# Kernel tuning notes

Measured on AMD Instinct MI355X. Metric: run time of the kernel, lower is better.

Reference implementation:

```python
import jax, jax.numpy as jnp
import numpy as np

N = 100000      # nodes
E = 1600000     # edges (before self-loops)
D_IN = 128      # node_attr_size
H = 4           # gat_heads
C = 32          # hidden_size (per-head out channels)
F = H * C       # feature_size = 128
K = 16          # num_clusters
L = 2           # num_gat_layers
EPS = 1e-5
NEG_SLOPE = 0.2  # PyG GATv2Conv default leaky_relu slope


def setup_inputs() -> dict:
    key = jax.random.key(0)
    ks = jax.random.split(key, 8)
    x = jax.random.normal(ks[0], (N, D_IN), jnp.float32)
    edge_index = jax.random.randint(ks[1], (2, E), 0, N, jnp.int32)
    sF = 1.0 / np.sqrt(F).astype(np.float32)
    Wp = jax.random.normal(ks[2], (D_IN, F), jnp.float32) * (1.0 / np.sqrt(D_IN).astype(np.float32))
    bp = jnp.zeros((F,), jnp.float32)
    ln_g = jnp.ones((L, F), jnp.float32)
    ln_b = jnp.zeros((L, F), jnp.float32)
    Wl = jax.random.normal(ks[3], (L, F, H * C), jnp.float32) * sF
    bl = jnp.zeros((L, H * C), jnp.float32)
    Wr = jax.random.normal(ks[4], (L, F, H * C), jnp.float32) * sF
    br = jnp.zeros((L, H * C), jnp.float32)
    att = jax.random.normal(ks[5], (L, H, C), jnp.float32) * (1.0 / np.sqrt(C).astype(np.float32))
    gb = jnp.zeros((L, F), jnp.float32)  # GATv2Conv output bias
    Wc = jax.random.normal(ks[6], (F, K), jnp.float32) * sF
    bc = jnp.zeros((K,), jnp.float32)
    return dict(x=x, edge_index=edge_index, Wp=Wp, bp=bp, ln_g=ln_g, ln_b=ln_b,
                Wl=Wl, bl=bl, Wr=Wr, br=br, att=att, gb=gb, Wc=Wc, bc=bc)


def _layernorm(x, g, b):
    mu = jnp.mean(x, axis=-1, keepdims=True)
    var = jnp.var(x, axis=-1, keepdims=True)
    return (x - mu) * jax.lax.rsqrt(var + EPS) * g + b


def reference(x, edge_index, Wp, bp, ln_g, ln_b, Wl, bl, Wr, br, att, gb, Wc, bc):
    # GATv2Conv adds self-loops by default
    loops = jnp.arange(N, dtype=edge_index.dtype)
    src = jnp.concatenate([edge_index[0], loops])  # message source j
    dst = jnp.concatenate([edge_index[1], loops])  # message target i

    h = x @ Wp + bp  # node_feat_proj -> [N, F]
    for i in range(L):
        identity = h
        hn = _layernorm(h, ln_g[i], ln_b[i])
        x_l = (hn @ Wl[i] + bl[i]).reshape(N, H, C)  # source transform
        x_r = (hn @ Wr[i] + br[i]).reshape(N, H, C)  # target transform
        m = x_l[src] + x_r[dst]                       # [E+N, H, C]
        s = jnp.where(m > 0, m, NEG_SLOPE * m)        # leaky_relu(0.2)
        logits = jnp.einsum('ehc,hc->eh', s, att[i])  # [E+N, H]
        # segment softmax over incoming edges of each target node
        mx = jax.ops.segment_max(logits, dst, num_segments=N)
        a = jnp.exp(logits - mx[dst])
        den = jax.ops.segment_sum(a, dst, num_segments=N)
        alpha = a / den[dst]
        out = jax.ops.segment_sum(x_l[src] * alpha[:, :, None], dst, num_segments=N)
        out = out.reshape(N, F) + gb[i]
        # relu activation, dropout identity (eval), residual add
        h = jax.nn.relu(out) + identity

    classification_output = h @ Wc + bc
    return (classification_output, h)
```

## Files before the change

kernel.cpp:

```cpp
#include <hip/hip_runtime.h>
#include <hip/hip_bf16.h>
#include <math.h>
#include <stdint.h>

#define N_NODES 100000
#define N_EDGES 1600000
#define ET (N_EDGES + N_NODES)
#define FDIM 128
#define NK 16
#define EPS 1e-5f
#define SLOPE 0.2f

typedef __attribute__((ext_vector_type(8))) short bf16x8;
typedef __attribute__((ext_vector_type(4))) float f32x4;
typedef __attribute__((ext_vector_type(2))) _Float16 h2;

__device__ inline unsigned pk_bf16(float a, float b) {
    float2 f; f.x = a; f.y = b;
    __hip_bfloat162 t = __float22bfloat162_rn(f);
    return *reinterpret_cast<unsigned*>(&t);
}
__device__ inline h2 as_h2(unsigned u) { return __builtin_bit_cast(h2, u); }
__device__ inline unsigned as_u(h2 v) { return __builtin_bit_cast(unsigned, v); }

#define SWZ(X, P) __int_as_float(__builtin_amdgcn_ds_swizzle(__float_as_int(X), (P)))
#define DPPF(X, CTRL) __int_as_float(__builtin_amdgcn_mov_dpp(__float_as_int(X), (CTRL), 0xF, 0xF, true))
#define DX1(X) DPPF(X, 0xB1)
#define DX2(X) DPPF(X, 0x4E)
#define DR4(X) DPPF(X, 0x124)
#define DR8(X) DPPF(X, 0x128)
#define DB0(X) DPPF(X, 0x00)
#define DB1(X) DPPF(X, 0x55)
#define DB2(X) DPPF(X, 0xAA)
#define DB3(X) DPPF(X, 0xFF)

__device__ inline float exp2_hw(float x) {
    float r;
    asm("v_exp_f32 %0, %1" : "=v"(r) : "v"(x));
    return r;
}

#define FMAMIX_LO(ACC, U, W) \
    asm("v_fma_mix_f32 %0, %1, %2, %0 op_sel_hi:[1,0,0]" : "+v"(ACC) : "v"(U), "v"(W))
#define FMAMIX_HI(ACC, U, W) \
    asm("v_fma_mix_f32 %0, %1, %2, %0 op_sel:[1,0,0] op_sel_hi:[1,0,0]" : "+v"(ACC) : "v"(U), "v"(W))

__device__ inline int rflm(int v) { return __builtin_amdgcn_readfirstlane(v) & 131071; }


#define NBKT 196
#define BSH 9
#define BSTRIDE 10240
#define P1_EPT 8
#define P1_EPB (256 * P1_EPT)
#define PART_BLOCKS ((ET + P1_EPB - 1) / P1_EPB)

__global__ __launch_bounds__(256) void prep_kernel(
        const int* __restrict__ ei, int* __restrict__ gcount,
        int* __restrict__ staging,
        const float* __restrict__ Wp, const float* __restrict__ Wl,
        const float* __restrict__ Wr, ushort* __restrict__ wbp,
        ushort* __restrict__ wbl0, ushort* __restrict__ wbl1) {
    __shared__ int hist[NBKT];
    __shared__ int lofs[NBKT];
    __shared__ int gbase[NBKT];
    __shared__ int s[256];
    __shared__ int spk[P1_EPB];
    __shared__ short sbk[P1_EPB];
    int bid = blockIdx.x;
    int t = threadIdx.x;
    if (bid >= PART_BLOCKS) {
        int bb = bid - PART_BLOCKS;
        const float *W0, *W1; ushort* out; int nt;
        if (bb < 8)       { W0 = Wp; W1 = Wp; out = wbp; nt = bb; }
        else if (bb < 24) { W0 = Wl; W1 = Wr; out = wbl0; nt = bb - 8; }
        else              { W0 = Wl + FDIM * FDIM; W1 = Wr + FDIM * FDIM; out = wbl1; nt = bb - 24; }
        int kk = t >> 6, lane = t & 63;
        int n = nt * 16 + (lane & 15);
        int k0 = kk * 32 + (lane >> 4) * 8;
        const float* W = (n < 128) ? (W0 + n) : (W1 + (n - 128));
        float f[8];
#pragma unroll
        for (int j = 0; j < 8; j++) f[j] = W[(size_t)(k0 + j) * FDIM];
        uint4 u;
        u.x = pk_bf16(f[0], f[1]); u.y = pk_bf16(f[2], f[3]);
        u.z = pk_bf16(f[4], f[5]); u.w = pk_bf16(f[6], f[7]);
        *(uint4*)&out[(size_t)((nt * 4 + kk) * 64 + lane) * 8] = u;
        return;
    }
    if (t < NBKT) hist[t] = 0;
    __syncthreads();
    int e0 = bid * P1_EPB + t;
    int pk[P1_EPT], bk[P1_EPT], rk[P1_EPT];
#pragma unroll
    for (int k = 0; k < P1_EPT; k++) {
        int e = e0 + k * 256;
        bk[k] = -1;
        if (e < ET) {
            int src, dst;
            if (e < N_EDGES) { src = ei[e]; dst = ei[N_EDGES + e]; }
            else             { src = dst = e - N_EDGES; }
            int b = dst >> BSH;
            pk[k] = (src << BSH) | (dst & 511);
            bk[k] = b;
            rk[k] = atomicAdd(&hist[b], 1);
        }
    }
    __syncthreads();
    int v = (t < NBKT) ? hist[t] : 0;
    s[t] = v;
    __syncthreads();
    for (int o = 1; o < 256; o <<= 1) {
        int add = (t >= o) ? s[t - o] : 0;
        __syncthreads();
        s[t] += add;
        __syncthreads();
    }
    if (t < NBKT) {
        lofs[t] = s[t] - v;
        gbase[t] = (v > 0) ? atomicAdd(&gcount[t], v) : 0;
    }
    __syncthreads();
#pragma unroll
    for (int k = 0; k < P1_EPT; k++) {
        if (bk[k] >= 0) {
            int idx = lofs[bk[k]] + rk[k];
            spk[idx] = pk[k];
            sbk[idx] = (short)bk[k];
        }
    }
    __syncthreads();
    int tot = lofs[NBKT - 1] + hist[NBKT - 1];
    for (int i = t; i < tot; i += 256) {
        int b = sbk[i];
        staging[b * BSTRIDE + gbase[b] + (i - lofs[b])] = spk[i];
    }
}

__global__ __launch_bounds__(256) void csr_projln_kernel(
        const int* __restrict__ staging, const int* __restrict__ gcount,
        int* __restrict__ off, int* __restrict__ perm,
        const float* __restrict__ x, const ushort* __restrict__ wb,
        const float* __restrict__ bp, float* __restrict__ h,
        const ushort* __restrict__ wbl,
        const float* __restrict__ g_, const float* __restrict__ b_,
        const float* __restrict__ bl, const float* __restrict__ br,
        ushort* __restrict__ xlh, ushort* __restrict__ xrh) {
    __shared__ uint4 fragbuf[4 * 272];
    int bid = blockIdx.x;
    int t = threadIdx.x;
    if (bid >= NBKT) {
        int wid = ((bid - NBKT) * 256 + t) >> 6;
        int lane = t & 63;
        if (wid >= N_NODES / 16) return;
        uint4* fb = fragbuf + (t >> 6) * 272;
        int q = lane >> 4, m = lane & 15;
        int row0 = wid * 16;
        const float* xrow = x + (size_t)(row0 + m) * FDIM + q * 32;
#pragma unroll
        for (int p = 0; p < 4; p++) {
            float4 a = *(const float4*)&xrow[p * 8];
            float4 c = *(const float4*)&xrow[p * 8 + 4];
            uint4 u;
            u.x = pk_bf16(a.x, a.y); u.y = pk_bf16(a.z, a.w);
            u.z = pk_bf16(c.x, c.y); u.w = pk_bf16(c.z, c.w);
            fb[q * 68 + p * 17 + m] = u;
        }
        bf16x8 A[4];
#pragma unroll
        for (int kk = 0; kk < 4; kk++)
            A[kk] = *(const bf16x8*)&fb[kk * 68 + q * 17 + m];
        const bf16x8* wbv = (const bf16x8*)wb;
        f32x4 acc[8];
        f32x4 z = {0.f, 0.f, 0.f, 0.f};
#pragma unroll
        for (int nt = 0; nt < 8; nt++) acc[nt] = z;
#pragma unroll
        for (int nt = 0; nt < 8; nt++) {
#pragma unroll
            for (int kk = 0; kk < 4; kk++) {
                bf16x8 B = wbv[(nt * 4 + kk) * 64 + lane];
                acc[nt] = __builtin_amdgcn_mfma_f32_16x16x32_bf16(A[kk], B, acc[nt], 0, 0, 0);
            }
        }
        float hv[8][4];
#pragma unroll
        for (int nt = 0; nt < 8; nt++) {
            int col = nt * 16 + m;
            float bias = bp[col];
#pragma unroll
            for (int r = 0; r < 4; r++) {
                hv[nt][r] = acc[nt][r] + bias;
                h[(size_t)(row0 + q * 4 + r) * FDIM + col] = hv[nt][r];
            }
        }
        if (!wbl) return;
        float gc[8], bcv[8];
#pragma unroll
        for (int nt = 0; nt < 8; nt++) { gc[nt] = g_[nt * 16 + m]; bcv[nt] = b_[nt * 16 + m]; }
        ushort* fbu = (ushort*)fb;
#pragma unroll
        for (int r = 0; r < 4; r++) {
            float s = 0.f, ss = 0.f;
#pragma unroll
            for (int nt = 0; nt < 8; nt++) { s += hv[nt][r]; ss += hv[nt][r] * hv[nt][r]; }
            s += SWZ(s, 0x041F); s += SWZ(s, 0x081F); s += SWZ(s, 0x101F); s += SWZ(s, 0x201F);
            ss += SWZ(ss, 0x041F); ss += SWZ(ss, 0x081F); ss += SWZ(ss, 0x101F); ss += SWZ(ss, 0x201F);
            float mu = s * (1.f / 128.f);
            float rv = rsqrtf(ss * (1.f / 128.f) - mu * mu + EPS);
#pragma unroll
            for (int nt = 0; nt < 8; nt++) {
                float val = (hv[nt][r] - mu) * rv * gc[nt] + bcv[nt];
                ushort us = (ushort)pk_bf16(val, val);
                fbu[(((nt >> 1) * 68 + ((nt & 1) * 2 + (m >> 3)) * 17 + (q * 4 + r)) << 3) + (m & 7)] = us;
            }
        }
        bf16x8 A2[4];
#pragma unroll
        for (int kk = 0; kk < 4; kk++)
            A2[kk] = *(const bf16x8*)&fb[kk * 68 + q * 17 + m];
        const bf16x8* wlv = (const bf16x8*)wbl;
        f32x4 acc2[16];
#pragma unroll
        for (int nt = 0; nt < 16; nt++) acc2[nt] = z;
#pragma unroll
        for (int nt = 0; nt < 16; nt++) {
#pragma unroll
            for (int kk = 0; kk < 4; kk++) {
                bf16x8 B = wlv[(nt * 4 + kk) * 64 + lane];
                acc2[nt] = __builtin_amdgcn_mfma_f32_16x16x32_bf16(A2[kk], B, acc2[nt], 0, 0, 0);
            }
        }
#pragma unroll
        for (int nt = 0; nt < 16; nt++) {
            int col = nt * 16 + m;
            if (nt < 8) {
                float bias = bl[col];
#pragma unroll
                for (int r = 0; r < 4; r++) {
                    _Float16 hf = (_Float16)(acc2[nt][r] + bias);
                    xlh[(size_t)(row0 + q * 4 + r) * FDIM + col] = __builtin_bit_cast(ushort, hf);
                }
            } else {
                int c2 = col - 128;
                float bias = br[c2];
#pragma unroll
                for (int r = 0; r < 4; r++) {
                    _Float16 hf = (_Float16)(acc2[nt][r] + bias);
                    xrh[(size_t)(row0 + q * 4 + r) * FDIM + c2] = __builtin_bit_cast(ushort, hf);
                }
            }
        }
        return;
    }
    int* hist = (int*)fragbuf;
    int* cur  = hist + 512;
    int* pr   = cur + 512;
    int* gpre = pr + 256;
    int b = bid;
    hist[t] = 0; hist[t + 256] = 0;
    gpre[t] = (t < NBKT) ? gcount[t] : 0;
    __syncthreads();
    int sz = gcount[b];
    for (int k = t; k < sz; k += 256)
        atomicAdd(&hist[staging[b * BSTRIDE + k] & 511], 1);
    __syncthreads();
    int a0 = hist[2 * t], a1 = hist[2 * t + 1];
    pr[t] = a0 + a1;
    __syncthreads();
    for (int o = 1; o < 256; o <<= 1) {
        int ad = (t >= o) ? pr[t - o] : 0;
        int gd = (t >= o) ? gpre[t - o] : 0;
        __syncthreads();
        pr[t] += ad;
        gpre[t] += gd;
        __syncthreads();
    }
    int base = gpre[b] - sz;
    int pe = pr[t] - (a0 + a1);
    cur[2 * t] = pe;
    cur[2 * t + 1] = pe + a0;
    int n = (b << BSH) + 2 * t;
    if (n < N_NODES)     off[n]     = base + pe;
    if (n + 1 < N_NODES) off[n + 1] = base + pe + a0;
    if (b == 0 && t == 0) off[N_NODES] = ET;
    __syncthreads();
    for (int k = t; k < sz; k += 256) {
        int p = staging[b * BSTRIDE + k];
        int slot = atomicAdd(&cur[p & 511], 1);
        perm[base + slot] = p >> BSH;
    }
}


__global__ __launch_bounds__(256) void ln_gemm2_kernel(
        const float* __restrict__ h,
        const float* __restrict__ g, const float* __restrict__ b,
        const ushort* __restrict__ wb, const float* __restrict__ bl,
        const float* __restrict__ br,
        ushort* __restrict__ xlh, ushort* __restrict__ xrh) {
    __shared__ uint4 fragbuf[4 * 272];
    int wid = (blockIdx.x * 256 + threadIdx.x) >> 6;
    int lane = threadIdx.x & 63;
    if (wid >= N_NODES / 16) return;
    uint4* fb = fragbuf + (threadIdx.x >> 6) * 272;
    int q = lane >> 4, m = lane & 15;
    int row0 = wid * 16;
    const float* hrow = h + (size_t)(row0 + m) * FDIM + q * 32;
    float v[32];
#pragma unroll
    for (int i = 0; i < 8; i++) {
        float4 t4 = *(const float4*)&hrow[i * 4];
        v[i * 4 + 0] = t4.x; v[i * 4 + 1] = t4.y; v[i * 4 + 2] = t4.z; v[i * 4 + 3] = t4.w;
    }
    float s = 0.f, ss = 0.f;
#pragma unroll
    for (int i = 0; i < 32; i++) { s += v[i]; ss += v[i] * v[i]; }
    s  += __shfl_xor(s, 16);  s  += __shfl_xor(s, 32);
    ss += __shfl_xor(ss, 16); ss += __shfl_xor(ss, 32);
    float mu = s * (1.f / 128.f);
    float var = ss * (1.f / 128.f) - mu * mu;
    float rv = rsqrtf(var + EPS);
#pragma unroll
    for (int i = 0; i < 8; i++) {
        float4 gv = *(const float4*)&g[q * 32 + i * 4];
        float4 bv = *(const float4*)&b[q * 32 + i * 4];
        v[i * 4 + 0] = (v[i * 4 + 0] - mu) * rv * gv.x + bv.x;
        v[i * 4 + 1] = (v[i * 4 + 1] - mu) * rv * gv.y + bv.y;
        v[i * 4 + 2] = (v[i * 4 + 2] - mu) * rv * gv.z + bv.z;
        v[i * 4 + 3] = (v[i * 4 + 3] - mu) * rv * gv.w + bv.w;
    }
#pragma unroll
    for (int p = 0; p < 4; p++) {
        uint4 u;
        u.x = pk_bf16(v[p * 8 + 0], v[p * 8 + 1]);
        u.y = pk_bf16(v[p * 8 + 2], v[p * 8 + 3]);
        u.z = pk_bf16(v[p * 8 + 4], v[p * 8 + 5]);
        u.w = pk_bf16(v[p * 8 + 6], v[p * 8 + 7]);
        fb[q * 68 + p * 17 + m] = u;
    }
    bf16x8 A[4];
#pragma unroll
    for (int kk = 0; kk < 4; kk++)
        A[kk] = *(const bf16x8*)&fb[kk * 68 + q * 17 + m];
    const bf16x8* wbv = (const bf16x8*)wb;
    f32x4 acc[16];
    f32x4 z = {0.f, 0.f, 0.f, 0.f};
#pragma unroll
    for (int nt = 0; nt < 16; nt++) acc[nt] = z;
#pragma unroll
    for (int nt = 0; nt < 16; nt++) {
#pragma unroll
        for (int kk = 0; kk < 4; kk++) {
            bf16x8 B = wbv[(nt * 4 + kk) * 64 + lane];
            acc[nt] = __builtin_amdgcn_mfma_f32_16x16x32_bf16(A[kk], B, acc[nt], 0, 0, 0);
        }
    }
#pragma unroll
    for (int nt = 0; nt < 16; nt++) {
        int col = nt * 16 + m;
        if (nt < 8) {
            float bias = bl[col];
#pragma unroll
            for (int r = 0; r < 4; r++) {
                _Float16 hf = (_Float16)(acc[nt][r] + bias);
                xlh[(size_t)(row0 + q * 4 + r) * FDIM + col] = __builtin_bit_cast(ushort, hf);
            }
        } else {
            int c2 = col - 128;
            float bias = br[c2];
#pragma unroll
            for (int r = 0; r < 4; r++) {
                _Float16 hf = (_Float16)(acc[nt][r] + bias);
                xrh[(size_t)(row0 + q * 4 + r) * FDIM + c2] = __builtin_bit_cast(ushort, hf);
            }
        }
    }
}


__global__ __launch_bounds__(256) void gat_agg_kernel(
        const unsigned* __restrict__ xlp, const unsigned* __restrict__ xrp,
        const int* __restrict__ off, const int* __restrict__ perm,
        const float* __restrict__ att, const float* __restrict__ gb,
        float* __restrict__ h,
        const float* __restrict__ Wc, const float* __restrict__ bc,
        float* __restrict__ out_cls) {
    __shared__ float WcS[FDIM * NK];
    __shared__ float hbuf[4 * 256];
    bool dofinal = (Wc != nullptr);
    if (dofinal) {
        for (int i = threadIdx.x; i < FDIM * NK; i += 256) WcS[i] = Wc[i];
        __syncthreads();
    }
    int wave = (blockIdx.x * 256 + threadIdx.x) >> 6;
    unsigned lane = threadIdx.x & 63;
    int iA = wave * 2;
    int iB = iA + 1;
    int2 oA = *(const int2*)&off[iA];
    int eB2 = off[iB + 1];
    h2 xrvA = as_h2(xrp[(unsigned)iA * 64u + lane]);
    h2 xrvB = as_h2(xrp[(unsigned)iB * 64u + lane]);
    const float2 hidA = *(const float2*)&h[(size_t)iA * FDIM + lane * 2];
    const float2 hidB = *(const float2*)&h[(size_t)iB * FDIM + lane * 2];
    const float2 gbv = *(const float2*)&gb[lane * 2];
    float2 attf = *(const float2*)&att[lane * 2];
    h2 attp; attp[0] = (_Float16)(attf.x * 1.44269504f);
    attp[1] = (_Float16)(attf.y * 1.44269504f);
    const h2 c06 = {(_Float16)0.6f, (_Float16)0.6f};
    const h2 c04 = {(_Float16)0.4f, (_Float16)0.4f};
    bool b0 = lane & 1, b1 = lane & 2;
    int begA = __builtin_amdgcn_readfirstlane(oA.x);
    int endA = __builtin_amdgcn_readfirstlane(oA.y);
    int begB = endA;
    int endB = __builtin_amdgcn_readfirstlane(eB2);
    const char* xlB_ = (const char*)xlp;
    unsigned laneB = lane << 2;

#define GLD(J) (*(const unsigned*)(xlB_ + ((unsigned)(J) * 256u + laneB)))

#define EDGE_PARTIAL(XRV, U, T)                                     \
    {                                                               \
        h2 mm = as_h2(U) + XRV;                                     \
        h2 am = as_h2(as_u(mm) & 0x7FFF7FFFu);                      \
        h2 sv = am * c04 + mm * c06;                                \
        T = __builtin_amdgcn_fdot2(sv, attp, 0.f, false);           \
    }

#define COMPUTE4(S, U0, U1, U2, U3)                                 \
    {                                                               \
        float t0, t1, t2, t3;                                       \
        EDGE_PARTIAL(xrv##S, U0, t0);                               \
        EDGE_PARTIAL(xrv##S, U1, t1);                               \
        EDGE_PARTIAL(xrv##S, U2, t2);                               \
        EDGE_PARTIAL(xrv##S, U3, t3);                               \
        float u   = b0 ? t1 : t0;                                   \
        float uu2 = b0 ? t0 : t1;                                   \
        u += DX1(uu2);                                              \
        float vv  = b0 ? t3 : t2;                                   \
        float vv2 = b0 ? t2 : t3;                                   \
        vv += DX1(vv2);                                             \
        float ww  = b1 ? vv : u;                                    \
        float ww2 = b1 ? u : vv;                                    \
        ww += DX2(ww2);                                             \
        ww += DR4(ww);                                              \
        ww += DR8(ww);                                              \
        float ew = exp2_hw(ww);                                     \
        dloc##S += ew;                                              \
        float w0 = DB0(ew);                                         \
        float w1 = DB1(ew);                                         \
        float w2 = DB2(ew);                                         \
        float w3 = DB3(ew);                                         \
        FMAMIX_LO(accx##S, U0, w0); FMAMIX_HI(accy##S, U0, w0);     \
        FMAMIX_LO(accx##S, U1, w1); FMAMIX_HI(accy##S, U1, w1);     \
        FMAMIX_LO(accx##S, U2, w2); FMAMIX_HI(accy##S, U2, w2);     \
        FMAMIX_LO(accx##S, U3, w3); FMAMIX_HI(accy##S, U3, w3);     \
    }

#define TAIL1(S, U)                                                 \
    {                                                               \
        float tt;                                                   \
        EDGE_PARTIAL(xrv##S, U, tt);                                \
        tt += DX1(tt);                                              \
        tt += DX2(tt);                                              \
        tt += DR4(tt);                                              \
        tt += DR8(tt);                                              \
        float w = exp2_hw(tt);                                      \
        if ((lane & 3) == 0) dloc##S += w;                          \
        FMAMIX_LO(accx##S, U, w); FMAMIX_HI(accy##S, U, w);         \
    }

    int nbA = (endA - begA) >> 2, tlA = (endA - begA) & 3;
    int nbB = (endB - begB) >> 2, tlB = (endB - begB) & 3;
    float accxA = 0.f, accyA = 0.f, dlocA = 0.f;
    float accxB = 0.f, accyB = 0.f, dlocB = 0.f;
    unsigned c0A, c1A, c2A, c3A, d0A, d1A, d2A, d3A; int4 p2A;
    unsigned c0B, c1B, c2B, c3B, d0B, d1B, d2B, d3B; int4 p2B;
    unsigned t0A = 0, t1A = 0, t2A = 0, t0B = 0, t1B = 0, t2B = 0;
    int4 p0A, p1A, ptA, p0B, p1B, ptB;

    if (nbA > 0) {
        __builtin_memcpy(&p0A, perm + begA, 16);
        __builtin_memcpy(&p1A, perm + begA + 4, 16);
        __builtin_memcpy(&p2A, perm + begA + 8, 16);
    }
    if (tlA > 0) __builtin_memcpy(&ptA, perm + begA + 4 * nbA, 16);
    if (nbB > 0) {
        __builtin_memcpy(&p0B, perm + begB, 16);
        __builtin_memcpy(&p1B, perm + begB + 4, 16);
        __builtin_memcpy(&p2B, perm + begB + 8, 16);
    }
    if (tlB > 0) __builtin_memcpy(&ptB, perm + begB + 4 * nbB, 16);
    if (nbA > 0) {
        c0A = GLD(rflm(p0A.x)); c1A = GLD(rflm(p0A.y)); c2A = GLD(rflm(p0A.z)); c3A = GLD(rflm(p0A.w));
        d0A = GLD(rflm(p1A.x)); d1A = GLD(rflm(p1A.y)); d2A = GLD(rflm(p1A.z)); d3A = GLD(rflm(p1A.w));
    }
    if (nbB > 0) {
        c0B = GLD(rflm(p0B.x)); c1B = GLD(rflm(p0B.y)); c2B = GLD(rflm(p0B.z)); c3B = GLD(rflm(p0B.w));
        d0B = GLD(rflm(p1B.x)); d1B = GLD(rflm(p1B.y)); d2B = GLD(rflm(p1B.z)); d3B = GLD(rflm(p1B.w));
    }
    if (tlA > 0) {
        t0A = GLD(rflm(ptA.x));
        if (tlA > 1) t1A = GLD(rflm(ptA.y));
        if (tlA > 2) t2A = GLD(rflm(ptA.z));
    }
    if (tlB > 0) {
        t0B = GLD(rflm(ptB.x));
        if (tlB > 1) t1B = GLD(rflm(ptB.y));
        if (tlB > 2) t2B = GLD(rflm(ptB.z));
    }

    int blkA = 0, blkB = 0;
    while (blkA + 2 < nbA && blkB + 2 < nbB) {
        unsigned e0 = GLD(rflm(p2A.x)), e1 = GLD(rflm(p2A.y));
        unsigned e2 = GLD(rflm(p2A.z)), e3 = GLD(rflm(p2A.w));
        unsigned f0 = GLD(rflm(p2B.x)), f1 = GLD(rflm(p2B.y));
        unsigned f2 = GLD(rflm(p2B.z)), f3 = GLD(rflm(p2B.w));
        __builtin_memcpy(&p2A, perm + begA + 4 * blkA + 12, 16);
        __builtin_memcpy(&p2B, perm + begB + 4 * blkB + 12, 16);
        COMPUTE4(A, c0A, c1A, c2A, c3A);
        c0A = d0A; c1A = d1A; c2A = d2A; c3A = d3A;
        d0A = e0; d1A = e1; d2A = e2; d3A = e3;
        COMPUTE4(B, c0B, c1B, c2B, c3B);
        c0B = d0B; c1B = d1B; c2B = d2B; c3B = d3B;
        d0B = f0; d1B = f1; d2B = f2; d3B = f3;
        ++blkA; ++blkB;
    }
    for (; blkA + 2 < nbA; ++blkA) {
        unsigned e0 = GLD(rflm(p2A.x)), e1 = GLD(rflm(p2A.y));
        unsigned e2 = GLD(rflm(p2A.z)), e3 = GLD(rflm(p2A.w));
        __builtin_memcpy(&p2A, perm + begA + 4 * blkA + 12, 16);
        COMPUTE4(A, c0A, c1A, c2A, c3A);
        c0A = d0A; c1A = d1A; c2A = d2A; c3A = d3A;
        d0A = e0; d1A = e1; d2A = e2; d3A = e3;
    }
    for (; blkB + 2 < nbB; ++blkB) {
        unsigned f0 = GLD(rflm(p2B.x)), f1 = GLD(rflm(p2B.y));
        unsigned f2 = GLD(rflm(p2B.z)), f3 = GLD(rflm(p2B.w));
        __builtin_memcpy(&p2B, perm + begB + 4 * blkB + 12, 16);
        COMPUTE4(B, c0B, c1B, c2B, c3B);
        c0B = d0B; c1B = d1B; c2B = d2B; c3B = d3B;
        d0B = f0; d1B = f1; d2B = f2; d3B = f3;
    }
    if (nbA >= 2) {
        COMPUTE4(A, c0A, c1A, c2A, c3A);
        c0A = d0A; c1A = d1A; c2A = d2A; c3A = d3A;
    }
    if (nbB >= 2) {
        COMPUTE4(B, c0B, c1B, c2B, c3B);
        c0B = d0B; c1B = d1B; c2B = d2B; c3B = d3B;
    }
    if (nbA >= 1) COMPUTE4(A, c0A, c1A, c2A, c3A);
    if (nbB >= 1) COMPUTE4(B, c0B, c1B, c2B, c3B);
    if (tlA > 0) {
        TAIL1(A, t0A);
        if (tlA > 1) TAIL1(A, t1A);
        if (tlA > 2) TAIL1(A, t2A);
    }
    if (tlB > 0) {
        TAIL1(B, t0B);
        if (tlB > 1) TAIL1(B, t1B);
        if (tlB > 2) TAIL1(B, t2B);
    }
#undef EDGE_PARTIAL
#undef COMPUTE4
#undef TAIL1
#undef GLD

    float denA = dlocA + DX1(dlocA);
    denA += DX2(denA);
    float invA = 1.f / denA;
    float2 resA;
    resA.x = fmaxf(accxA * invA + gbv.x, 0.f) + hidA.x;
    resA.y = fmaxf(accyA * invA + gbv.y, 0.f) + hidA.y;
    *(float2*)&h[(size_t)iA * FDIM + lane * 2] = resA;
    float denB = dlocB + DX1(dlocB);
    denB += DX2(denB);
    float invB = 1.f / denB;
    float2 resB;
    resB.x = fmaxf(accxB * invB + gbv.x, 0.f) + hidB.x;
    resB.y = fmaxf(accyB * invB + gbv.y, 0.f) + hidB.y;
    *(float2*)&h[(size_t)iB * FDIM + lane * 2] = resB;

    if (dofinal) {
        float* sh = hbuf + (threadIdx.x >> 6) * 256;
        sh[lane * 2]       = resA.x; sh[lane * 2 + 1]       = resA.y;
        sh[128 + lane * 2] = resB.x; sh[128 + lane * 2 + 1] = resB.y;
        int k = lane & 15, g = lane >> 4;
        float pA = 0.f, pB = 0.f;
#pragma unroll 8
        for (int c = g * 32; c < g * 32 + 32; ++c) {
            float wv = WcS[c * NK + k];
            pA = fmaf(sh[c], wv, pA);
            pB = fmaf(sh[128 + c], wv, pB);
        }
        pA += SWZ(pA, 0x401F);
        pB += SWZ(pB, 0x401F);
        pA += __shfl_xor(pA, 32);
        pB += __shfl_xor(pB, 32);
        if (g == 0) {
            float bk = bc[k];
            out_cls[(size_t)iA * NK + k] = pA + bk;
            out_cls[(size_t)iB * NK + k] = pB + bk;
        }
    }
}


extern "C" void kernel_launch(void* const* d_in, const int* in_sizes, int n_in,
                              void* d_out, int out_size, void* d_ws, size_t ws_size,
                              hipStream_t stream) {
    const float* x    = (const float*)d_in[0];
    const int*   ei   = (const int*)  d_in[1];
    const float* Wp   = (const float*)d_in[2];
    const float* bp   = (const float*)d_in[3];
    const float* ln_g = (const float*)d_in[4];
    const float* ln_b = (const float*)d_in[5];
    const float* Wl   = (const float*)d_in[6];
    const float* bl   = (const float*)d_in[7];
    const float* Wr   = (const float*)d_in[8];
    const float* br   = (const float*)d_in[9];
    const float* att  = (const float*)d_in[10];
    const float* gb   = (const float*)d_in[11];
    const float* Wc   = (const float*)d_in[12];
    const float* bc   = (const float*)d_in[13];

    float* out_cls = (float*)d_out;
    float* h = out_cls + (size_t)N_NODES * NK;

    char* w = (char*)d_ws;
    int* off    = (int*)w; w += (size_t)(N_NODES + 1) * sizeof(int);
    int* gcount = (int*)w; w += 256 * sizeof(int);
    int* perm   = (int*)w; w += (size_t)ET * sizeof(int);
    uintptr_t a = ((uintptr_t)w + 255) & ~(uintptr_t)255;
    ushort* xlh = (ushort*)a;
    ushort* xrh = xlh + (size_t)N_NODES * FDIM;
    ushort* wbp = xrh + (size_t)N_NODES * FDIM;
    ushort* wbl0 = wbp + 8 * 4 * 64 * 8;
    ushort* wbl1 = wbl0 + 16 * 4 * 64 * 8;
    char* wend = (char*)(wbl1 + 16 * 4 * 64 * 8);
    size_t need = (size_t)(wend - (char*)d_ws) + (size_t)NBKT * BSTRIDE * sizeof(int);
    bool roomy = (ws_size >= need);
    int* staging = roomy ? (int*)wend : (int*)xlh;

    hipMemsetAsync(gcount, 0, NBKT * sizeof(int), stream);
    prep_kernel<<<PART_BLOCKS + 40, 256, 0, stream>>>(
        ei, gcount, staging, Wp, Wl, Wr, wbp, wbl0, wbl1);
    const int gw = (N_NODES / 16 + 3) / 4;
    csr_projln_kernel<<<NBKT + gw, 256, 0, stream>>>(
        staging, gcount, off, perm, x, wbp, bp, h,
        roomy ? wbl0 : (const ushort*)nullptr,
        ln_g, ln_b, bl, br, xlh, xrh);
    if (!roomy)
        ln_gemm2_kernel<<<gw, 256, 0, stream>>>(
            h, ln_g, ln_b, wbl0, bl, br, xlh, xrh);

    gat_agg_kernel<<<(N_NODES / 2) / 4, 256, 0, stream>>>(
        (const unsigned*)xlh, (const unsigned*)xrh, off, perm,
        att, gb, h, nullptr, nullptr, nullptr);
    ln_gemm2_kernel<<<gw, 256, 0, stream>>>(
        h, ln_g + FDIM, ln_b + FDIM, wbl1, bl + FDIM, br + FDIM, xlh, xrh);
    gat_agg_kernel<<<(N_NODES / 2) / 4, 256, 0, stream>>>(
        (const unsigned*)xlh, (const unsigned*)xrh, off, perm,
        att + FDIM, gb + FDIM, h, Wc, bc, out_cls);
}
```

Measured before the change: 391.7 us.

## Fuse layer-2 LayerNorm and Wl/Wr GEMM into layer-1 aggregation epilogue

The first GAT aggregation kernel now computes LayerNorm of its output rows in registers, stages them as bf16 in shared memory, and runs the 16x256 MFMA projection to produce layer-2 xl/xr directly. This removes the separate ln_gemm2 launch and its re-read of h. Blocks grow to 512 threads (16 nodes per block) so each block owns a full MFMA tile. The outputs go to separate workspace buffers so in-flight readers of the layer-1 xl/xr are not overwritten. The change adds register and LDS pressure, plus a block-wide sync, to the aggregation kernel.

```diff
diff --git a/kernel.cpp b/kernel.cpp
--- a/kernel.cpp
+++ b/kernel.cpp
@@ -33,6 +33,8 @@
 #define DB1(X) DPPF(X, 0x55)
 #define DB2(X) DPPF(X, 0xAA)
 #define DB3(X) DPPF(X, 0xFF)
+#define RED64(S) { S += DX1(S); S += DX2(S); S += DR4(S); S += DR8(S); \
+                   S += SWZ(S, 0x401F); S += __shfl_xor(S, 32); }
 
 __device__ inline float exp2_hw(float x) {
     float r;
@@ -379,21 +381,25 @@
 }
 
 
-__global__ __launch_bounds__(256) void gat_agg_kernel(
+__global__ __launch_bounds__(512) void gat_agg_kernel(
         const unsigned* __restrict__ xlp, const unsigned* __restrict__ xrp,
         const int* __restrict__ off, const int* __restrict__ perm,
         const float* __restrict__ att, const float* __restrict__ gb,
         float* __restrict__ h,
         const float* __restrict__ Wc, const float* __restrict__ bc,
-        float* __restrict__ out_cls) {
+        float* __restrict__ out_cls,
+        const ushort* __restrict__ wbl,
+        const float* __restrict__ lgp, const float* __restrict__ lbp,
+        const float* __restrict__ bl1, const float* __restrict__ br1,
+        ushort* __restrict__ xl1, ushort* __restrict__ xr1) {
     __shared__ float WcS[FDIM * NK];
-    __shared__ float hbuf[4 * 256];
+    __shared__ float hbuf[8 * 256];
     bool dofinal = (Wc != nullptr);
     if (dofinal) {
-        for (int i = threadIdx.x; i < FDIM * NK; i += 256) WcS[i] = Wc[i];
+        for (int i = threadIdx.x; i < FDIM * NK; i += 512) WcS[i] = Wc[i];
         __syncthreads();
     }
-    int wave = (blockIdx.x * 256 + threadIdx.x) >> 6;
+    int wave = (blockIdx.x * 512 + threadIdx.x) >> 6;
     unsigned lane = threadIdx.x & 63;
     int iA = wave * 2;
     int iB = iA + 1;
@@ -589,7 +595,8 @@
         int k = lane & 15, g = lane >> 4;
         float pA = 0.f, pB = 0.f;
 #pragma unroll 8
-        for (int c = g * 32; c < g * 32 + 32; ++c) {
+        for (int i = 0; i < 32; ++i) {
+            int c = 4 * i + g;
             float wv = WcS[c * NK + k];
             pA = fmaf(sh[c], wv, pA);
             pB = fmaf(sh[128 + c], wv, pB);
@@ -602,6 +609,63 @@
             float bk = bc[k];
             out_cls[(size_t)iA * NK + k] = pA + bk;
             out_cls[(size_t)iB * NK + k] = pB + bk;
+        }
+    }
+
+    if (xl1) {
+        float sA = resA.x + resA.y, qsA = resA.x * resA.x + resA.y * resA.y;
+        float sB = resB.x + resB.y, qsB = resB.x * resB.x + resB.y * resB.y;
+        RED64(sA); RED64(qsA); RED64(sB); RED64(qsB);
+        float muA = sA * (1.f / 128.f);
+        float rvA = rsqrtf(qsA * (1.f / 128.f) - muA * muA + EPS);
+        float muB = sB * (1.f / 128.f);
+        float rvB = rsqrtf(qsB * (1.f / 128.f) - muB * muB + EPS);
+        float2 lgv = *(const float2*)&lgp[lane * 2];
+        float2 lbv = *(const float2*)&lbp[lane * 2];
+        unsigned* fb32 = (unsigned*)WcS;
+        int w = threadIdx.x >> 6;
+        int fbase = ((int)(lane >> 4) * 68 + (int)((lane >> 2) & 3) * 17) * 4 + (int)(lane & 3);
+        fb32[fbase + (2 * w) * 4] =
+            pk_bf16((resA.x - muA) * rvA * lgv.x + lbv.x,
+                    (resA.y - muA) * rvA * lgv.y + lbv.y);
+        fb32[fbase + (2 * w + 1) * 4] =
+            pk_bf16((resB.x - muB) * rvB * lgv.x + lbv.x,
+                    (resB.y - muB) * rvB * lgv.y + lbv.y);
+        __syncthreads();
+        const uint4* fbq = (const uint4*)WcS;
+        int q = lane >> 4, m = lane & 15;
+        bf16x8 A2[4];
+#pragma unroll
+        for (int kk = 0; kk < 4; kk++)
+            A2[kk] = *(const bf16x8*)&fbq[kk * 68 + q * 17 + m];
+        const bf16x8* wlv = (const bf16x8*)wbl;
+        int row0 = blockIdx.x * 16;
+        f32x4 z = {0.f, 0.f, 0.f, 0.f};
+#pragma unroll
+        for (int tt = 0; tt < 2; ++tt) {
+            int nt = 2 * w + tt;
+            f32x4 acc2 = z;
+#pragma unroll
+            for (int kk = 0; kk < 4; kk++)
+                acc2 = __builtin_amdgcn_mfma_f32_16x16x32_bf16(
+                    A2[kk], wlv[(nt * 4 + kk) * 64 + lane], acc2, 0, 0, 0);
+            int col = nt * 16 + m;
+            if (nt < 8) {
+                float bias = bl1[col];
+#pragma unroll
+                for (int r = 0; r < 4; r++) {
+                    _Float16 hf = (_Float16)(acc2[r] + bias);
+                    xl1[(size_t)(row0 + q * 4 + r) * FDIM + col] = __builtin_bit_cast(ushort, hf);
+                }
+            } else {
+                int c2 = col - 128;
+                float bias = br1[c2];
+#pragma unroll
+                for (int r = 0; r < 4; r++) {
+                    _Float16 hf = (_Float16)(acc2[r] + bias);
+                    xr1[(size_t)(row0 + q * 4 + r) * FDIM + c2] = __builtin_bit_cast(ushort, hf);
+                }
+            }
         }
     }
 }
@@ -639,9 +703,14 @@
     ushort* wbl0 = wbp + 8 * 4 * 64 * 8;
     ushort* wbl1 = wbl0 + 16 * 4 * 64 * 8;
     char* wend = (char*)(wbl1 + 16 * 4 * 64 * 8);
-    size_t need = (size_t)(wend - (char*)d_ws) + (size_t)NBKT * BSTRIDE * sizeof(int);
-    bool roomy = (ws_size >= need);
+    size_t base_need = (size_t)(wend - (char*)d_ws);
+    size_t stag_sz = (size_t)NBKT * BSTRIDE * sizeof(int);
+    size_t xlr1_sz = (size_t)2 * N_NODES * FDIM * sizeof(ushort);
+    bool roomy  = (ws_size >= base_need + stag_sz);
+    bool roomy2 = (ws_size >= base_need + stag_sz + xlr1_sz);
     int* staging = roomy ? (int*)wend : (int*)xlh;
+    ushort* xlh1 = roomy2 ? (ushort*)((char*)wend + stag_sz) : nullptr;
+    ushort* xrh1 = roomy2 ? xlh1 + (size_t)N_NODES * FDIM : nullptr;
 
     hipMemsetAsync(gcount, 0, NBKT * sizeof(int), stream);
     prep_kernel<<<PART_BLOCKS + 40, 256, 0, stream>>>(
@@ -655,12 +724,18 @@
         ln_gemm2_kernel<<<gw, 256, 0, stream>>>(
             h, ln_g, ln_b, wbl0, bl, br, xlh, xrh);
 
-    gat_agg_kernel<<<(N_NODES / 2) / 4, 256, 0, stream>>>(
+    gat_agg_kernel<<<N_NODES / 16, 512, 0, stream>>>(
         (const unsigned*)xlh, (const unsigned*)xrh, off, perm,
-        att, gb, h, nullptr, nullptr, nullptr);
-    ln_gemm2_kernel<<<gw, 256, 0, stream>>>(
-        h, ln_g + FDIM, ln_b + FDIM, wbl1, bl + FDIM, br + FDIM, xlh, xrh);
-    gat_agg_kernel<<<(N_NODES / 2) / 4, 256, 0, stream>>>(
-        (const unsigned*)xlh, (const unsigned*)xrh, off, perm,
-        att + FDIM, gb + FDIM, h, Wc, bc, out_cls);
+        att, gb, h, nullptr, nullptr, nullptr,
+        roomy2 ? wbl1 : (const ushort*)nullptr,
+        ln_g + FDIM, ln_b + FDIM, bl + FDIM, br + FDIM, xlh1, xrh1);
+    if (!roomy2)
+        ln_gemm2_kernel<<<gw, 256, 0, stream>>>(
+            h, ln_g + FDIM, ln_b + FDIM, wbl1, bl + FDIM, br + FDIM, xlh, xrh);
+    const ushort* xl_1 = roomy2 ? xlh1 : xlh;
+    const ushort* xr_1 = roomy2 ? xrh1 : xrh;
+    gat_agg_kernel<<<N_NODES / 16, 512, 0, stream>>>(
+        (const unsigned*)xl_1, (const unsigned*)xr_1, off, perm,
+        att + FDIM, gb + FDIM, h, Wc, bc, out_cls,
+        nullptr, nullptr, nullptr, nullptr, nullptr, nullptr, nullptr);
 }
```

New measurement: 399.1 us. No clear change (+1.9%).
